# Kernel tuning notes

Measured on AMD Instinct MI355X. Metric: run time of the kernel, lower is better.

Reference implementation:

```python
import jax, jax.numpy as jnp
import numpy as np
from jax.experimental import sparse as jsparse

N_ITEMS = 20000   # item catalog size (S is [N_ITEMS, N_ITEMS])
N_USERS = 2048    # user batch
NNZ = 4_000_000


def setup_inputs() -> dict:
    key = jax.random.key(0)
    k1, k2, k3, k4 = jax.random.split(key, 4)
    X = jax.random.normal(k1, (N_USERS, N_ITEMS), dtype=jnp.float32)
    S_vals = jax.random.normal(k2, (NNZ,), dtype=jnp.float32)
    S_rows = jax.random.randint(k3, (NNZ,), 0, N_ITEMS, dtype=jnp.int32)
    S_cols = jax.random.randint(k4, (NNZ,), 0, N_ITEMS, dtype=jnp.int32)
    return {"X": X, "S_vals": S_vals, "S_rows": S_rows, "S_cols": S_cols}


def reference(X, S_vals, S_rows, S_cols):
    # torch.sparse.mm(S, X.t()).t()  ==  X @ S^T, with S sparse COO.
    indices = jnp.stack([S_rows, S_cols], axis=1)  # [nnz, 2]
    S = jsparse.BCOO((S_vals, indices), shape=(N_ITEMS, N_ITEMS))
    # (S @ X^T)^T -> [n_users, n_items]; duplicate indices sum, matching COO semantics.
    return (S @ X.T).T
```

## Files before the change

### kernel.cpp

```cpp
#include <hip/hip_runtime.h>

#define N_ITEMS 20000
#define N_USERS 2048
#define NNZ     4000000
#define LDP     2112
#define HALF_ITEMS 10000
#define CAP_H   192

typedef float    f32x4 __attribute__((ext_vector_type(4)));
typedef unsigned u32x4 __attribute__((ext_vector_type(4)));

#define OFF_XT     ((size_t)0)
#define OFF_CSRPK  ((size_t)84480000)
#define OFF_CNT    (OFF_CSRPK + 30720000)

static __device__ __forceinline__ unsigned short f2bf(float f) {
  unsigned u = __float_as_uint(f);
  unsigned r = (u + 0x7fffu + ((u >> 16) & 1u)) >> 16;
  return (unsigned short)r;
}

__global__ __launch_bounds__(256) void transpose_kernel(
    const float* __restrict__ X, unsigned short* __restrict__ XT) {
  __shared__ float tile[64][65];
  int k0 = blockIdx.x * 64;
  int u0 = blockIdx.y * 64;
  int lane = threadIdx.x & 63;
  int dq = threadIdx.x >> 6;
  #pragma unroll
  for (int m = 0; m < 16; ++m) {
    int u = u0 + dq + 4 * m;
    int k = k0 + lane;
    float v = 0.f;
    if (k < N_ITEMS) v = X[(size_t)u * N_ITEMS + k];
    tile[lane][dq + 4 * m] = v;
  }
  __syncthreads();
  #pragma unroll
  for (int m = 0; m < 16; ++m) {
    int k = k0 + dq + 4 * m;
    if (k < N_ITEMS)
      XT[(size_t)k * LDP + u0 + lane] = f2bf(tile[dq + 4 * m][lane]);
  }
}

__global__ __launch_bounds__(256) void scatter_kernel(
    const int* __restrict__ rows, const int* __restrict__ cols,
    const float* __restrict__ vals, int* __restrict__ cnt,
    unsigned* __restrict__ csr_pk) {
  int i = blockIdx.x * 256 + threadIdx.x;
  int r = rows[i];
  int c = cols[i];
  float v = vals[i];
  int h = (c >= HALF_ITEMS) ? 1 : 0;
  int bin = 2 * r + h;
  int pos = atomicAdd(&cnt[bin], 1);
  if (pos >= CAP_H) pos = CAP_H - 1;
  csr_pk[bin * CAP_H + pos] =
      ((unsigned)(c - h * HALF_ITEMS) << 16) | (unsigned)f2bf(v);
}

__global__ __launch_bounds__(256) void spmm_kernel(
    const int* __restrict__ cnt, const unsigned* __restrict__ csr_pk,
    const unsigned short* __restrict__ xt, float* __restrict__ out,
    int uc, int h) {
  __shared__ float tile[8][132];
  int wg = blockIdx.x;
  int xcd = wg & 7;
  int rb = wg >> 3;
  int u0 = (xcd * 2 + uc) * 128;
  int r0 = rb * 8;
  int lane = threadIdx.x & 63;
  int wave = __builtin_amdgcn_readfirstlane((int)(threadIdx.x >> 6));
  unsigned lane4 = 4 * (unsigned)lane;
  const char* xtb = (const char*)(xt + (size_t)h * HALF_ITEMS * LDP + u0);
  int ul = threadIdx.x >> 1;
  int rhalf = (threadIdx.x & 1) * 4;
  float* op = out + (size_t)(u0 + ul) * N_ITEMS + r0 + rhalf;

#define LOAD8(E, BASE)                                                       \
  { u32x4 q0 = __builtin_nontemporal_load(                                   \
        reinterpret_cast<const u32x4*>(csr_pk + (BASE)));                    \
    u32x4 q1 = __builtin_nontemporal_load(                                   \
        reinterpret_cast<const u32x4*>(csr_pk + (BASE) + 4));                \
    E[0] = q0.x; E[1] = q0.y; E[2] = q0.z; E[3] = q0.w;                      \
    E[4] = q1.x; E[5] = q1.y; E[6] = q1.z; E[7] = q1.w; }
#define GATHER8(G, E)                                                        \
  { _Pragma("unroll")                                                        \
    for (int k = 0; k < 8; ++k)                                              \
      G[k] = *reinterpret_cast<const unsigned*>(                             \
          xtb + ((E[k] >> 16) * (unsigned)(LDP * 2) + lane4)); }
#define FMA8(G, E)                                                           \
  { _Pragma("unroll")                                                        \
    for (int k = 0; k < 8; ++k) {                                            \
      float v  = __uint_as_float(E[k] << 16);                \
      float xl = __uint_as_float(G[k] << 16);                                \
      float xh = __uint_as_float(G[k]);                 \
      if (k & 1) { a2 = fmaf(v, xl, a2); a3 = fmaf(v, xh, a3); }             \
      else       { a0 = fmaf(v, xl, a0); a1 = fmaf(v, xh, a1); }             \
    } }

  if (h) {
    f32x4 i0 = __builtin_nontemporal_load(reinterpret_cast<const f32x4*>(op));
    tile[rhalf + 0][ul] = i0.x; tile[rhalf + 1][ul] = i0.y;
    tile[rhalf + 2][ul] = i0.z; tile[rhalf + 3][ul] = i0.w;
    __syncthreads();
  }

  #pragma unroll 1
  for (int rr = 0; rr < 2; ++rr) {
    int r = r0 + wave * 2 + rr;
    int bin = 2 * r + h;
    int jb = bin * CAP_H;
    int cr = __builtin_amdgcn_readfirstlane(cnt[bin]);
    if (cr > CAP_H) cr = CAP_H;
    int nb = (cr + 7) >> 3;
    float a0 = 0.f, a1 = 0.f, a2 = 0.f, a3 = 0.f;
    if (h) {
      a0 = tile[wave * 2 + rr][2 * lane];
      a1 = tile[wave * 2 + rr][2 * lane + 1];
    }
    if (nb >= 3) {
      unsigned e0[8], e1[8], e2[8], g0[8], g1[8], g2[8];
      LOAD8(e0, jb)
      GATHER8(g0, e0)
      LOAD8(e1, jb + 8)
      GATHER8(g1, e1)
      LOAD8(e2, jb + 16)
      int b = 0;
      for (; b + 5 < nb; b += 3) {
        GATHER8(g2, e2)
        FMA8(g0, e0)
        LOAD8(e0, jb + (b + 3) * 8)
        GATHER8(g0, e0)
        FMA8(g1, e1)
        LOAD8(e1, jb + (b + 4) * 8)
        GATHER8(g1, e1)
        FMA8(g2, e2)
        LOAD8(e2, jb + (b + 5) * 8)
      }
      int m = nb - b;
      GATHER8(g2, e2)
      FMA8(g0, e0)
      if (m == 3) {
        FMA8(g1, e1)
        FMA8(g2, e2)
      } else if (m == 4) {
        LOAD8(e0, jb + (b + 3) * 8)
        GATHER8(g0, e0)
        FMA8(g1, e1)
        FMA8(g2, e2)
        FMA8(g0, e0)
      } else {
        LOAD8(e0, jb + (b + 3) * 8)
        GATHER8(g0, e0)
        FMA8(g1, e1)
        LOAD8(e1, jb + (b + 4) * 8)
        GATHER8(g1, e1)
        FMA8(g2, e2)
        FMA8(g0, e0)
        FMA8(g1, e1)
      }
    } else if (nb == 2) {
      unsigned e0[8], e1[8], g0[8], g1[8];
      LOAD8(e0, jb)
      GATHER8(g0, e0)
      LOAD8(e1, jb + 8)
      GATHER8(g1, e1)
      FMA8(g0, e0)
      FMA8(g1, e1)
    } else if (nb == 1) {
      unsigned e0[8], g0[8];
      LOAD8(e0, jb)
      GATHER8(g0, e0)
      FMA8(g0, e0)
    }
    tile[wave * 2 + rr][2 * lane]     = a0 + a2;
    tile[wave * 2 + rr][2 * lane + 1] = a1 + a3;
  }
#undef LOAD8
#undef GATHER8
#undef FMA8

  __syncthreads();
  f32x4 o;
  o.x = tile[rhalf + 0][ul]; o.y = tile[rhalf + 1][ul];
  o.z = tile[rhalf + 2][ul]; o.w = tile[rhalf + 3][ul];
  __builtin_nontemporal_store(o, reinterpret_cast<f32x4*>(op));
}

extern "C" void kernel_launch(void* const* d_in, const int* in_sizes, int n_in,
                              void* d_out, int out_size, void* d_ws, size_t ws_size,
                              hipStream_t stream) {
  const float* X      = (const float*)d_in[0];
  const float* S_vals = (const float*)d_in[1];
  const int*   S_rows = (const int*)d_in[2];
  const int*   S_cols = (const int*)d_in[3];
  float* out = (float*)d_out;

  char* ws = (char*)d_ws;
  unsigned short* XT = (unsigned short*)(ws + OFF_XT);
  unsigned* csr_pk   = (unsigned*)(ws + OFF_CSRPK);
  int* cnt           = (int*)(ws + OFF_CNT);

  hipMemsetAsync(cnt, 0, 2 * N_ITEMS * sizeof(int), stream);
  hipMemsetAsync(csr_pk, 0, (size_t)2 * N_ITEMS * CAP_H * sizeof(unsigned), stream);
  transpose_kernel<<<dim3(313, 32), 256, 0, stream>>>(X, XT);
  scatter_kernel<<<NNZ / 256, 256, 0, stream>>>(S_rows, S_cols, S_vals, cnt, csr_pk);
  for (int p = 0; p < 4; ++p)
    spmm_kernel<<<2500 * 8, 256, 0, stream>>>(cnt, csr_pk, XT, out,
                                              p >> 1, p & 1);
}
```

Measured before the change: 1.040 ms.

## Split COO scatter into row-half passes and fuse second pass with transpose

The scatter now runs in two passes, each handling only the rows in one half of the item range, with vectorized nontemporal loads of four COO entries per thread. The second pass is fused into a single launch with the X transpose/bf16 conversion, so atomics over a smaller bin range overlap with the bandwidth-bound transpose. The aim is to reduce atomic contention and cache footprint of the scattered writes and to overlap scatter with transpose. The trade-off is reading the COO arrays twice and adding branch divergence in the scatter loop.

```diff
diff --git a/kernel.cpp b/kernel.cpp
--- a/kernel.cpp
+++ b/kernel.cpp
@@ -8,6 +8,7 @@
 #define CAP_H   192
 
 typedef float    f32x4 __attribute__((ext_vector_type(4)));
+typedef int      i32x4 __attribute__((ext_vector_type(4)));
 typedef unsigned u32x4 __attribute__((ext_vector_type(4)));
 
 #define OFF_XT     ((size_t)0)
@@ -20,44 +21,76 @@
   return (unsigned short)r;
 }
 
-__global__ __launch_bounds__(256) void transpose_kernel(
-    const float* __restrict__ X, unsigned short* __restrict__ XT) {
-  __shared__ float tile[64][65];
-  int k0 = blockIdx.x * 64;
-  int u0 = blockIdx.y * 64;
-  int lane = threadIdx.x & 63;
-  int dq = threadIdx.x >> 6;
-  #pragma unroll
-  for (int m = 0; m < 16; ++m) {
-    int u = u0 + dq + 4 * m;
-    int k = k0 + lane;
-    float v = 0.f;
-    if (k < N_ITEMS) v = X[(size_t)u * N_ITEMS + k];
-    tile[lane][dq + 4 * m] = v;
-  }
-  __syncthreads();
-  #pragma unroll
-  for (int m = 0; m < 16; ++m) {
-    int k = k0 + dq + 4 * m;
-    if (k < N_ITEMS)
-      XT[(size_t)k * LDP + u0 + lane] = f2bf(tile[dq + 4 * m][lane]);
-  }
-}
-
-__global__ __launch_bounds__(256) void scatter_kernel(
+#define NSQ ((NNZ / 4 + 255) / 256)
+#define NT_BLOCKS (313 * 32)
+
+static __device__ __forceinline__ void scatter_body(
+    const int* __restrict__ rows, const int* __restrict__ cols,
+    const float* __restrict__ vals, int* __restrict__ cnt,
+    unsigned* __restrict__ csr_pk, int pass, int b) {
+  int i = (b * 256 + (int)threadIdx.x) * 4;
+  if (i < NNZ) {
+    i32x4 r4 = __builtin_nontemporal_load(reinterpret_cast<const i32x4*>(rows + i));
+    i32x4 c4 = __builtin_nontemporal_load(reinterpret_cast<const i32x4*>(cols + i));
+    f32x4 v4 = __builtin_nontemporal_load(reinterpret_cast<const f32x4*>(vals + i));
+    #pragma unroll
+    for (int k = 0; k < 4; ++k) {
+      int r = r4[k];
+      if ((unsigned)(r - pass * HALF_ITEMS) < (unsigned)HALF_ITEMS) {
+        int c = c4[k];
+        float v = v4[k];
+        int h = (c >= HALF_ITEMS) ? 1 : 0;
+        int bin = 2 * r + h;
+        int pos = atomicAdd(&cnt[bin], 1);
+        if (pos >= CAP_H) pos = CAP_H - 1;
+        csr_pk[bin * CAP_H + pos] =
+            ((unsigned)(c - h * HALF_ITEMS) << 16) | (unsigned)f2bf(v);
+      }
+    }
+  }
+}
+
+__global__ __launch_bounds__(256) void scatterA_kernel(
     const int* __restrict__ rows, const int* __restrict__ cols,
     const float* __restrict__ vals, int* __restrict__ cnt,
     unsigned* __restrict__ csr_pk) {
-  int i = blockIdx.x * 256 + threadIdx.x;
-  int r = rows[i];
-  int c = cols[i];
-  float v = vals[i];
-  int h = (c >= HALF_ITEMS) ? 1 : 0;
-  int bin = 2 * r + h;
-  int pos = atomicAdd(&cnt[bin], 1);
-  if (pos >= CAP_H) pos = CAP_H - 1;
-  csr_pk[bin * CAP_H + pos] =
-      ((unsigned)(c - h * HALF_ITEMS) << 16) | (unsigned)f2bf(v);
+  scatter_body(rows, cols, vals, cnt, csr_pk, 0, blockIdx.x);
+}
+
+__global__ __launch_bounds__(256) void prepB_kernel(
+    const float* __restrict__ X, const int* __restrict__ rows,
+    const int* __restrict__ cols, const float* __restrict__ vals,
+    unsigned short* __restrict__ XT, int* __restrict__ cnt,
+    unsigned* __restrict__ csr_pk) {
+  int b = blockIdx.x;
+  if (b < NSQ) {
+    scatter_body(rows, cols, vals, cnt, csr_pk, 1, b);
+  } else {
+    __shared__ float tile[64][65];
+    int b2 = b - NSQ;
+    int k0 = (b2 % 313) * 64;
+    int u0 = (b2 / 313) * 64;
+    int lane = threadIdx.x & 63;
+    int dq = threadIdx.x >> 6;
+    #pragma unroll
+    for (int m = 0; m < 16; ++m) {
+      int u = u0 + dq + 4 * m;
+      int k = k0 + lane;
+      float v = 0.f;
+      if (k < N_ITEMS)
+        v = __builtin_nontemporal_load(&X[(size_t)u * N_ITEMS + k]);
+      tile[lane][dq + 4 * m] = v;
+    }
+    __syncthreads();
+    #pragma unroll
+    for (int m = 0; m < 16; ++m) {
+      int k = k0 + dq + 4 * m;
+      if (k < N_ITEMS) {
+        unsigned short s = f2bf(tile[dq + 4 * m][lane]);
+        __builtin_nontemporal_store(s, &XT[(size_t)k * LDP + u0 + lane]);
+      }
+    }
+  }
 }
 
 __global__ __launch_bounds__(256) void spmm_kernel(
@@ -205,8 +238,9 @@
 
   hipMemsetAsync(cnt, 0, 2 * N_ITEMS * sizeof(int), stream);
   hipMemsetAsync(csr_pk, 0, (size_t)2 * N_ITEMS * CAP_H * sizeof(unsigned), stream);
-  transpose_kernel<<<dim3(313, 32), 256, 0, stream>>>(X, XT);
-  scatter_kernel<<<NNZ / 256, 256, 0, stream>>>(S_rows, S_cols, S_vals, cnt, csr_pk);
+  scatterA_kernel<<<NSQ, 256, 0, stream>>>(S_rows, S_cols, S_vals, cnt, csr_pk);
+  prepB_kernel<<<NSQ + NT_BLOCKS, 256, 0, stream>>>(
+      X, S_rows, S_cols, S_vals, XT, cnt, csr_pk);
   for (int p = 0; p < 4; ++p)
     spmm_kernel<<<2500 * 8, 256, 0, stream>>>(cnt, csr_pk, XT, out,
                                               p >> 1, p & 1);
```

Result: slower. 1.082 ms (+4.1%).
